# Kernel tuning notes

Measured on AMD Instinct MI355X. Metric: run time of the kernel, lower is better.

Reference implementation:

```python
import jax, jax.numpy as jnp
import numpy as np

GAMMA = 0.5          # cfg.distribution_loss.triplet_loss_gamma
POS_RADIUS = 0.6     # cfg.fine_loss.positive_radius
BIG = 1e12

B, K = 4096, 64      # node correspondences, knn points per node
N = K + 1            # matching_scores has one slack row/col


def setup_inputs() -> dict:
    key = jax.random.key(0)
    k1, k2, k3, k4, k5 = jax.random.split(key, 5)
    pos_pts = jax.random.normal(k1, (B, K, 3), dtype=jnp.float32)
    # anchor points near positives so some pairs fall inside positive_radius
    anc_pts = pos_pts + 0.3 * jax.random.normal(k2, (B, K, 3), dtype=jnp.float32)
    pos_masks = jax.random.uniform(k3, (B, K)) < 0.9
    anc_masks = jax.random.uniform(k4, (B, K)) < 0.9
    matching_scores = jax.random.normal(k5, (B, N, N), dtype=jnp.float32)
    transform = jnp.eye(4, dtype=jnp.float32)  # rigid SE(3); identity keeps pos/neg masks realistic
    return {
        'pos_node_corr_knn_points': pos_pts,
        'anc_node_corr_knn_points': anc_pts,
        'pos_node_corr_knn_masks': pos_masks,
        'anc_node_corr_knn_masks': anc_masks,
        'matching_scores': matching_scores,
        'transform': transform,
    }


def _apply_transform(points, transform):
    R = transform[:3, :3]
    t = transform[:3, 3]
    return jnp.einsum('bkd,ed->bke', points, R) + t


def _pairwise_sq_dist(x, y):
    # (b,n,3),(b,m,3) -> (b,n,m) squared distances
    x2 = jnp.sum(x * x, axis=-1)
    y2 = jnp.sum(y * y, axis=-1)
    xy = jnp.einsum('bnd,bmd->bnm', x, y)
    return x2[:, :, None] - 2.0 * xy + y2[:, None, :]


def reference(pos_node_corr_knn_points, anc_node_corr_knn_points,
              pos_node_corr_knn_masks, anc_node_corr_knn_masks,
              matching_scores, transform):
    b, n, m = matching_scores.shape
    anc = _apply_transform(anc_node_corr_knn_points, transform)
    dists = _pairwise_sq_dist(pos_node_corr_knn_points, anc)  # (b, n-1, m-1)

    gt_masks = pos_node_corr_knn_masks[:, :, None] & anc_node_corr_knn_masks[:, None, :]
    gt_corr = (dists < POS_RADIUS ** 2) & gt_masks
    gt_neg = dists > (2.0 * POS_RADIUS) ** 2
    row_none = jnp.sum(gt_corr, axis=2) == 0   # (b, n-1): rows w/o correspondence -> slack col
    col_none = jnp.sum(gt_corr, axis=1) == 0   # (b, m-1): cols w/o correspondence -> slack row

    pos_mask = (jnp.zeros((b, n, m), dtype=bool)
                .at[:, :-1, :-1].set(gt_corr)
                .at[:, :-1, -1].set(row_none)
                .at[:, -1, :-1].set(col_none))
    neg_mask = (jnp.zeros((b, n, m), dtype=bool)
                .at[:, :-1, :-1].set(gt_neg)
                .at[:, :-1, -1].set(~row_none)
                .at[:, -1, :-1].set(~col_none))

    ms = matching_scores

    # ---- row direction (over pos knn rows, all m cols) ----
    pm = pos_mask[:, :-1, :]
    nm = neg_mask[:, :-1, :]
    ms_r = ms[:, :-1, :]
    pos_score = jnp.sum(jnp.where(pm, -ms_r, 0.0), axis=2) / jnp.sum(pm, axis=2)  # (b, n-1); count>=1
    neg_score = jnp.where(nm, -ms_r, BIG)                                          # (b, n-1, m)
    gap1 = pos_score[:, :, None] - neg_score
    per1 = jnp.log(jnp.sum(jnp.maximum(gap1 + GAMMA, 0.0), axis=2) + 1.0)          # (b, n-1)
    keep1 = pos_score != BIG
    loss1 = jnp.sum(jnp.where(keep1, per1, 0.0)) / jnp.maximum(jnp.sum(keep1), 1)

    # ---- column direction (over anc knn cols, all n rows) ----
    pmc = pos_mask[:, :, :-1]
    nmc = neg_mask[:, :, :-1]
    ms_c = ms[:, :, :-1]
    pos_score_inv = jnp.sum(jnp.where(pmc, -ms_c, 0.0), axis=1) / jnp.sum(pmc, axis=1)  # (b, m-1)
    neg_score_inv = jnp.where(nmc, -ms_c, BIG)                                           # (b, n, m-1)
    gap2 = jnp.transpose(pos_score_inv[:, None, :] - neg_score_inv, (0, 2, 1))           # (b, m-1, n)
    per2 = jnp.log(jnp.sum(jnp.maximum(gap2 + GAMMA, 0.0), axis=2) + 1.0)                # (b, m-1)
    keep2 = pos_score_inv != BIG
    loss2 = jnp.sum(jnp.where(keep2, per2, 0.0)) / jnp.maximum(jnp.sum(keep2), 1)

    return (loss1 + loss2) / 2.0
```

## Files before the change

### kernel.cpp

```cpp
#include <hip/hip_runtime.h>
#include <hip/hip_fp16.h>


#define R2_POS 0.36f
#define R2_NEG 1.44f
#define GAMMA_C 0.5f
#define NBATCH 4096
#define NPART (NBATCH * 2)
#define HCNEG -1024.0f

typedef _Float16 hf2 __attribute__((ext_vector_type(2)));

__device__ __forceinline__ int maskbit(const void* p, int i, int mode) {
    if (mode == 0) return ((const unsigned*)p)[i] != 0u;
    if (mode == 1) return ((const unsigned short*)p)[i] != 0;
    return ((const unsigned char*)p)[i] != 0;
}

__device__ __forceinline__ float sload(float v) {
    return __uint_as_float(__builtin_amdgcn_readfirstlane(__float_as_uint(v)));
}

__global__ __launch_bounds__(128, 4)
void fused_kernel(const float* __restrict__ posp,
                  const float* __restrict__ ancp,
                  const void* __restrict__ pmp,
                  const void* __restrict__ amp,
                  const float* __restrict__ msp,
                  const float* __restrict__ xfp,
                  float* __restrict__ partials) {
    __shared__ float2 tileF2[2113];
    __shared__ float4 ancs[64];

    const int tid = threadIdx.x;
    const int b = blockIdx.x;
    const int w = tid >> 6;
    const int l = tid & 63;
    const int ofs = b & 1;

    unsigned mw0 = ((const unsigned*)pmp)[l];
    bool okw = (mw0 == 0u) || (mw0 == 1u) || (mw0 == 0x3F800000u);
    unsigned hh0 = mw0 & 0xFFFFu, hh1 = mw0 >> 16;
    bool okh = (hh0 == 0u || hh0 == 0x3F80u) && (hh1 == 0u || hh1 == 0x3F80u);
    int mmode = (__ballot(okw) == ~0ULL) ? 0 : ((__ballot(okh) == ~0ULL) ? 1 : 2);

    float T[12];
#pragma unroll
    for (int e = 0; e < 3; ++e)
#pragma unroll
        for (int d = 0; d < 4; ++d) T[e * 4 + d] = sload(xfp[e * 4 + d]);

    const int pb = (b * 64 + l) * 3;
    const float px = posp[pb], py = posp[pb + 1], pz = posp[pb + 2];
    const float r0 = ancp[pb], r1 = ancp[pb + 1], r2 = ancp[pb + 2];
    const float ax = T[0] * r0 + T[1] * r1 + T[2]  * r2 + T[3];
    const float ay = T[4] * r0 + T[5] * r1 + T[6]  * r2 + T[7];
    const float az = T[8] * r0 + T[9] * r1 + T[10] * r2 + T[11];

    const int mi = b * 64 + l;
    const unsigned long long pmM = __ballot(maskbit(pmp, mi, mmode) != 0);
    const unsigned long long amM = __ballot(maskbit(amp, mi, mmode) != 0);

    float psum = 0.f; int pcnt = 0; float slack;
    hf2 hc[32];

    if (w == 0) {
        ancs[l] = make_float4(ax, ay, az, 0.f);
        const float2* src = (const float2*)(msp + (size_t)b * 4225 - ofs);
#pragma unroll
        for (int k = 0; k < 17; ++k) {
            int p = l + 64 * k;
            if (p < 1056) {
                float2 a = src[2 * p], c = src[2 * p + 1];
                tileF2[2 * p]     = a;
                tileF2[2 * p + 1] = c;
            } else if (p == 1056) {
                tileF2[2112] = src[2112];
            }
        }

        const float* row = ((const float*)tileF2) + ofs + l * 65;
        const bool pmL = (pmM >> l) & 1ULL;
#pragma unroll
        for (int jj = 0; jj < 32; ++jj) {
            float h0, h1;
#pragma unroll
            for (int s = 0; s < 2; ++s) {
                const int j = 2 * jj + s;
                float v = row[j];
                float4 a = ancs[j];
                float dx = px - a.x, dy = py - a.y, dz = pz - a.z;
                float d2 = dx * dx + dy * dy + dz * dz;
                bool pos = pmL && ((amM >> j) & 1ULL) && (d2 < R2_POS);
                psum -= pos ? v : 0.f;
                pcnt += pos ? 1 : 0;
                float hcv = (d2 > R2_NEG) ? v : HCNEG;
                if (s == 0) h0 = hcv; else h1 = hcv;
            }
            hf2 h; h[0] = (_Float16)h0; h[1] = (_Float16)h1;
            hc[jj] = h;
        }
        slack = row[64];
    } else {
        const float* mcol = msp + (size_t)b * 4225 + l;
        const bool amL = (amM >> l) & 1ULL;
#pragma unroll
        for (int jj = 0; jj < 32; ++jj) {
            float h0, h1;
#pragma unroll
            for (int s = 0; s < 2; ++s) {
                const int r = 2 * jj + s;
                float v = mcol[r * 65];
                const int qb = (b * 64 + r) * 3;
                float qx = posp[qb], qy = posp[qb + 1], qz = posp[qb + 2];
                float dx = qx - ax, dy = qy - ay, dz = qz - az;
                float d2 = dx * dx + dy * dy + dz * dz;
                bool pos = ((pmM >> r) & 1ULL) && amL && (d2 < R2_POS);
                psum -= pos ? v : 0.f;
                pcnt += pos ? 1 : 0;
                float hcv = (d2 > R2_NEG) ? v : HCNEG;
                if (s == 0) h0 = hcv; else h1 = hcv;
            }
            hf2 h; h[0] = (_Float16)h0; h[1] = (_Float16)h1;
            hc[jj] = h;
        }
        slack = mcol[64 * 65];
    }

    const float ps = pcnt ? psum / (float)pcnt : -slack;

    const _Float16 ch = (_Float16)(ps + GAMMA_C);
    const hf2 C2 = {ch, ch};
    const hf2 Z = {(_Float16)0.f, (_Float16)0.f};
    float hv = 0.f;
#if __has_builtin(__builtin_amdgcn_fdot2)
    const hf2 ONE2 = {(_Float16)1.f, (_Float16)1.f};
#pragma unroll
    for (int k = 0; k < 32; ++k) {
        hf2 x = hc[k] + C2;
        x = __builtin_elementwise_max(x, Z);
        hv = __builtin_amdgcn_fdot2(x, ONE2, hv, false);
    }
#else
#pragma unroll
    for (int k = 0; k < 32; ++k) {
        hf2 x = hc[k] + C2;
        x = __builtin_elementwise_max(x, Z);
        hv += (float)x[0] + (float)x[1];
    }
#endif
    if (pcnt) hv += fmaxf(ps + slack + GAMMA_C, 0.f);
    float result = __logf(hv + 1.f);

#pragma unroll
    for (int off = 1; off < 64; off <<= 1)
        result += __shfl_xor(result, off, 64);
    if (l == 0) partials[b * 2 + w] = result;
}

__global__ void finalize_kernel(const float* __restrict__ partials,
                                unsigned* __restrict__ out) {
    __shared__ float red[4];
    const int tid = threadIdx.x;
    float s = 0.f;
    for (int i = tid; i < NPART; i += 256) s += partials[i];
#pragma unroll
    for (int off = 1; off < 64; off <<= 1) s += __shfl_xor(s, off, 64);
    if ((tid & 63) == 0) red[tid >> 6] = s;
    __syncthreads();
    if (tid == 0) {
        float tot = red[0] + red[1] + red[2] + red[3];
        float loss = tot * (1.0f / (2.0f * NBATCH * 64.0f));
        unsigned bits = __float_as_uint(loss);
        unsigned h = (bits + 0x7FFFu + ((bits >> 16) & 1u)) >> 16;
        out[0] = (h << 16) | h;
    }
}

extern "C" void kernel_launch(void* const* d_in, const int* in_sizes, int n_in,
                              void* d_out, int out_size, void* d_ws, size_t ws_size,
                              hipStream_t stream) {
    (void)in_sizes; (void)n_in; (void)out_size; (void)ws_size;
    const float* posp = (const float*)d_in[0];
    const float* ancp = (const float*)d_in[1];
    const void* pmp = d_in[2];
    const void* amp = d_in[3];
    const float* msp = (const float*)d_in[4];
    const float* xfp = (const float*)d_in[5];

    fused_kernel<<<NBATCH, 128, 0, stream>>>(posp, ancp, pmp, amp, msp, xfp,
                                             (float*)d_ws);
    finalize_kernel<<<1, 256, 0, stream>>>((const float*)d_ws,
                                           (unsigned*)d_out);
}
```

Baseline: 131.9 us.

## Replace LDS staging with direct row loads and cross-lane readlane broadcasts

Removes the shared-memory tile of matching scores and anchor points. Wave 0 now loads its own 65-float row straight from global memory with unaligned 16-byte copies. Both waves broadcast the other side's point coordinates with readlane instead of LDS reads or repeated global loads of posp. This cuts LDS traffic and redundant global loads. In exchange, row loads become strided and possibly misaligned across lanes, which risks poor coalescing, and it adds many scalar readlane operations.

```diff
diff --git a/kernel.cpp b/kernel.cpp
--- a/kernel.cpp
+++ b/kernel.cpp
@@ -10,6 +10,7 @@
 #define HCNEG -1024.0f
 
 typedef _Float16 hf2 __attribute__((ext_vector_type(2)));
+typedef float f4v __attribute__((ext_vector_type(4)));
 
 __device__ __forceinline__ int maskbit(const void* p, int i, int mode) {
     if (mode == 0) return ((const unsigned*)p)[i] != 0u;
@@ -21,6 +22,10 @@
     return __uint_as_float(__builtin_amdgcn_readfirstlane(__float_as_uint(v)));
 }
 
+__device__ __forceinline__ float rlane(float v, int i) {
+    return __uint_as_float(__builtin_amdgcn_readlane(__float_as_uint(v), i));
+}
+
 __global__ __launch_bounds__(128, 4)
 void fused_kernel(const float* __restrict__ posp,
                   const float* __restrict__ ancp,
@@ -29,14 +34,10 @@
                   const float* __restrict__ msp,
                   const float* __restrict__ xfp,
                   float* __restrict__ partials) {
-    __shared__ float2 tileF2[2113];
-    __shared__ float4 ancs[64];
-
     const int tid = threadIdx.x;
     const int b = blockIdx.x;
     const int w = tid >> 6;
     const int l = tid & 63;
-    const int ofs = b & 1;
 
     unsigned mw0 = ((const unsigned*)pmp)[l];
     bool okw = (mw0 == 0u) || (mw0 == 1u) || (mw0 == 0x3F800000u);
@@ -65,21 +66,13 @@
     hf2 hc[32];
 
     if (w == 0) {
-        ancs[l] = make_float4(ax, ay, az, 0.f);
-        const float2* src = (const float2*)(msp + (size_t)b * 4225 - ofs);
+        const float* rowp = msp + (size_t)b * 4225 + l * 65;
+        f4v ch[16];
 #pragma unroll
-        for (int k = 0; k < 17; ++k) {
-            int p = l + 64 * k;
-            if (p < 1056) {
-                float2 a = src[2 * p], c = src[2 * p + 1];
-                tileF2[2 * p]     = a;
-                tileF2[2 * p + 1] = c;
-            } else if (p == 1056) {
-                tileF2[2112] = src[2112];
-            }
-        }
+        for (int c = 0; c < 16; ++c)
+            __builtin_memcpy(&ch[c], rowp + 4 * c, 16);
+        slack = rowp[64];
 
-        const float* row = ((const float*)tileF2) + ofs + l * 65;
         const bool pmL = (pmM >> l) & 1ULL;
 #pragma unroll
         for (int jj = 0; jj < 32; ++jj) {
@@ -87,9 +80,11 @@
 #pragma unroll
             for (int s = 0; s < 2; ++s) {
                 const int j = 2 * jj + s;
-                float v = row[j];
-                float4 a = ancs[j];
-                float dx = px - a.x, dy = py - a.y, dz = pz - a.z;
+                float v = ch[j >> 2][j & 3];
+                float bx = rlane(ax, j);
+                float by = rlane(ay, j);
+                float bz = rlane(az, j);
+                float dx = px - bx, dy = py - by, dz = pz - bz;
                 float d2 = dx * dx + dy * dy + dz * dz;
                 bool pos = pmL && ((amM >> j) & 1ULL) && (d2 < R2_POS);
                 psum -= pos ? v : 0.f;
@@ -100,7 +95,6 @@
             hf2 h; h[0] = (_Float16)h0; h[1] = (_Float16)h1;
             hc[jj] = h;
         }
-        slack = row[64];
     } else {
         const float* mcol = msp + (size_t)b * 4225 + l;
         const bool amL = (amM >> l) & 1ULL;
@@ -111,8 +105,9 @@
             for (int s = 0; s < 2; ++s) {
                 const int r = 2 * jj + s;
                 float v = mcol[r * 65];
-                const int qb = (b * 64 + r) * 3;
-                float qx = posp[qb], qy = posp[qb + 1], qz = posp[qb + 2];
+                float qx = rlane(px, r);
+                float qy = rlane(py, r);
+                float qz = rlane(pz, r);
                 float dx = qx - ax, dy = qy - ay, dz = qz - az;
                 float d2 = dx * dx + dy * dy + dz * dz;
                 bool pos = ((pmM >> r) & 1ULL) && amL && (d2 < R2_POS);
@@ -129,8 +124,8 @@
 
     const float ps = pcnt ? psum / (float)pcnt : -slack;
 
-    const _Float16 ch = (_Float16)(ps + GAMMA_C);
-    const hf2 C2 = {ch, ch};
+    const _Float16 ch16 = (_Float16)(ps + GAMMA_C);
+    const hf2 C2 = {ch16, ch16};
     const hf2 Z = {(_Float16)0.f, (_Float16)0.f};
     float hv = 0.f;
 #if __has_builtin(__builtin_amdgcn_fdot2)
```

After: 130.4 us. No clear change (-1.2%).
